# Performance work log

Measured on AMD Instinct MI355X. Metric: run time of the kernel, lower is better.

## Reference

```python
import jax, jax.numpy as jnp
import numpy as np

NC = 65536   # candidate centers across FPN levels (single image)
NP = 1024    # proposal boxes == points
D = 256      # points_feat_dim
C = 256      # in_channels (query/key dim)
START_LEVEL = 3
NEG = -1e30


def setup_inputs() -> dict:
    key = jax.random.key(0)
    ks = jax.random.split(key, 9)
    # centers: [y, x, size, stride]; stride in {8,16,32,64,128} -> lvl 0..4
    lvl = jax.random.randint(ks[0], (NC,), 0, 5)
    stride = (2.0 ** (lvl + START_LEVEL)).astype(jnp.float32)
    yx = jax.random.uniform(ks[1], (NC, 2), minval=0.0, maxval=1024.0)
    centers = jnp.concatenate([yx, stride[:, None], stride[:, None]], axis=1)
    # boxes: [x1, y1, x2, y2]
    x1y1 = jax.random.uniform(ks[2], (NP, 2), minval=0.0, maxval=900.0)
    wh = jax.random.uniform(ks[3], (NP, 2), minval=64.0, maxval=256.0)
    boxes = jnp.concatenate([x1y1, x1y1 + wh], axis=1)
    points_feat = jax.random.normal(ks[4], (NP, D), dtype=jnp.float32)
    box_feat = jax.random.normal(ks[5], (NC, D), dtype=jnp.float32)
    Wq = jax.random.normal(ks[6], (D, C), dtype=jnp.float32) / np.sqrt(D).astype(np.float32)
    bq = jnp.zeros((C,), dtype=jnp.float32)
    Wk = jax.random.normal(ks[7], (D, C), dtype=jnp.float32) / np.sqrt(D).astype(np.float32)
    bk = jnp.zeros((C,), dtype=jnp.float32)
    scales = 1.0 + 0.1 * jax.random.normal(ks[8], (5,), dtype=jnp.float32)
    return dict(points_feat=points_feat, box_feat=box_feat, centers=centers,
                boxes=boxes, Wq=Wq, bq=bq, Wk=Wk, bk=bk, scales=scales)


def reference(points_feat, box_feat, centers, boxes, Wq, bq, Wk, bk, scales):
    # geometry -> containment mask [NC, NP] (center c inside box p)
    coord = centers[:, :2] + jnp.floor_divide(centers[:, 2:3], 2.0)  # [NC,2]
    ys, xs = coord[:, 0], coord[:, 1]
    l = xs[:, None] - boxes[None, :, 0]
    t = ys[:, None] - boxes[None, :, 1]
    r = boxes[None, :, 2] - xs[:, None]
    b = boxes[None, :, 3] - ys[:, None]
    mask = jnp.minimum(jnp.minimum(l, t), jnp.minimum(r, b)) > 0     # [NC,NP]

    stride = centers[:, 3]
    lvl = (jnp.log2(stride) - START_LEVEL).astype(jnp.int32)         # [NC] in 0..4
    w = scales[lvl]                                                  # per-level scale

    query = points_feat @ Wq + bq                                    # [NP,C]
    keyf = (box_feat * w[:, None]) @ Wk + bk                         # [NC,C]

    sim = jnp.clip(keyf @ query.T, -50.0, 50.0)                      # [NC,NP]
    logits = jnp.where(mask, sim, NEG)
    attn = jax.nn.softmax(logits, axis=0)
    attn = jnp.where(mask, attn, 0.0)                                # zero out invalid
    merge = attn.T @ box_feat                                        # [NP,D]
    return points_feat + merge
```

## Files before the change

kernel.cpp:

```cpp
#include <hip/hip_runtime.h>

typedef unsigned short ushort_t;
typedef _Float16 half8 __attribute__((ext_vector_type(8)));
typedef short short8 __attribute__((ext_vector_type(8)));
typedef float floatx4 __attribute__((ext_vector_type(4)));

#define NCC 65536
#define NPP 1024
#define DD 256
#define NCHUNK 64
#define VROW 36
#define VTILE_B (256 * VROW * 2)

static __device__ __forceinline__ ushort_t f2h_bits(float x) {
  _Float16 h = (_Float16)x;
  return __builtin_bit_cast(ushort_t, h);
}
static __device__ __forceinline__ ushort_t f2bf_bits(float x) {
  unsigned u = __builtin_bit_cast(unsigned, x);
  unsigned r = (u + 0x7FFFu + ((u >> 16) & 1u)) >> 16;
  return (ushort_t)r;
}

static __device__ __forceinline__ void dma16(const void* g, void* l) {
  __builtin_amdgcn_global_load_lds((const __attribute__((address_space(1))) unsigned int*)g,
                                   (__attribute__((address_space(3))) unsigned int*)l, 16, 0, 0);
}

static __device__ __forceinline__ short8 mk_s8(uint2 lo, uint2 hi) {
  uint4 u;
  u.x = lo.x; u.y = lo.y; u.z = hi.x; u.w = hi.y;
  return __builtin_bit_cast(short8, u);
}

__global__ __launch_bounds__(256) void wt_prep(const float* __restrict__ Wq,
                                               const float* __restrict__ Wk,
                                               ushort_t* __restrict__ WqT,
                                               ushort_t* __restrict__ WkT) {
  __shared__ __align__(16) ushort_t lt[64][80];
  const float* W = blockIdx.y ? Wk : Wq;
  ushort_t* WT = blockIdx.y ? WkT : WqT;
  const int k0 = ((int)blockIdx.x & 3) * 64, n0 = ((int)blockIdx.x >> 2) * 64;
  const int t = threadIdx.x;
#pragma unroll
  for (int i = 0; i < 4; i++) {
    int f = t + 256 * i;
    int k = f >> 4, j = (f & 15) * 4;
    const float4 v = *(const float4*)&W[(size_t)(k0 + k) * DD + n0 + j];
    lt[j + 0][k] = f2h_bits(v.x);
    lt[j + 1][k] = f2h_bits(v.y);
    lt[j + 2][k] = f2h_bits(v.z);
    lt[j + 3][k] = f2h_bits(v.w);
  }
  __syncthreads();
#pragma unroll
  for (int i = 0; i < 2; i++) {
    int f = t + 256 * i;
    int nl = f >> 3, grp = f & 7;
    int n = n0 + nl;
    int kp = k0 + ((grp ^ (n & 7)) * 8);
    *(uint4*)&WT[(size_t)n * DD + kp] = *(const uint4*)&lt[nl][grp * 8];
  }
}

__global__ __launch_bounds__(256) void prep_gemm(
    const float* __restrict__ box_feat, const float* __restrict__ points_feat,
    const float* __restrict__ centers, const float* __restrict__ scales,
    const ushort_t* __restrict__ WqT, const ushort_t* __restrict__ WkT,
    const float* __restrict__ bq, const float* __restrict__ bk,
    ushort_t* __restrict__ q_out, ushort_t* __restrict__ kf_out,
    float2* __restrict__ xy) {
  __shared__ __align__(16) ushort_t lds_a[64][264];
  __shared__ __align__(16) ushort_t lds_b[64 * 256];
  __shared__ __align__(16) ushort_t lds_o[64][72];
  __shared__ float lds_s[64];

  const int t = threadIdx.x;
  const bool isQ = (blockIdx.x >= (NCC / 64));
  const int row0 = isQ ? ((int)blockIdx.x - NCC / 64) * 64 : (int)blockIdx.x * 64;
  const float* In = isQ ? points_feat : box_feat;
  const ushort_t* WT = isQ ? WqT : WkT;
  const float* Bi = isQ ? bq : bk;
  ushort_t* Out = isQ ? q_out : kf_out;
  const int swz = isQ ? 0 : 7;

  if (t < 64) {
    float s = 1.0f;
    if (!isQ) {
      int c = row0 + t;
      float stride = centers[c * 4 + 3];
      int lvl = (int)(log2f(stride) + 0.5f) - 3;
      lvl = lvl < 0 ? 0 : (lvl > 4 ? 4 : lvl);
      s = scales[lvl];
      float hf = floorf(centers[c * 4 + 2] * 0.5f);
      xy[c] = make_float2(centers[c * 4 + 1] + hf, centers[c * 4 + 0] + hf);
    }
    lds_s[t] = s;
  }
  __syncthreads();

#pragma unroll
  for (int i = 0; i < 16; i++) {
    int f = t + 256 * i;
    int r = f >> 6;
    int c4 = (f & 63) * 4;
    const float4 v = *(const float4*)&In[(size_t)(row0 + r) * DD + c4];
    float s = lds_s[r];
    ushort_t h0 = f2h_bits(v.x * s), h1 = f2h_bits(v.y * s);
    ushort_t h2 = f2h_bits(v.z * s), h3 = f2h_bits(v.w * s);
    *(uint2*)&lds_a[r][c4] =
        make_uint2((unsigned)h0 | ((unsigned)h1 << 16), (unsigned)h2 | ((unsigned)h3 << 16));
  }

  const int w = t >> 6, lane = t & 63, qd = lane >> 4, n = lane & 15;
  const int sw8 = (n & 7) * 8;

  for (int g = 0; g < 4; ++g) {
    __syncthreads();
#pragma unroll
    for (int j = 0; j < 8; ++j) {
      int sg = w * 8 + j;
      dma16(&WT[(size_t)g * 64 * DD + sg * 512 + lane * 8], &lds_b[sg * 512 + lane * 8]);
    }
    __syncthreads();

    floatx4 acc[4] = {};
#pragma unroll
    for (int s = 0; s < 8; s++) {
      half8 af = __builtin_bit_cast(half8, *(const uint4*)&lds_a[w * 16 + n][s * 32 + qd * 8]);
      int off = (s * 32 + qd * 8) ^ sw8;
#pragma unroll
      for (int nt = 0; nt < 4; ++nt) {
        half8 bf = __builtin_bit_cast(half8, *(const uint4*)&lds_b[(nt * 16 + n) * 256 + off]);
        acc[nt] = __builtin_amdgcn_mfma_f32_16x16x32_f16(af, bf, acc[nt], 0, 0, 0);
      }
    }
#pragma unroll
    for (int nt = 0; nt < 4; ++nt) {
      float b = Bi[g * 64 + nt * 16 + n];
#pragma unroll
      for (int r = 0; r < 4; r++) lds_o[w * 16 + qd * 4 + r][nt * 16 + n] = f2h_bits(acc[nt][r] + b);
    }
    __syncthreads();
#pragma unroll
    for (int i = 0; i < 2; i++) {
      int idx = t * 2 + i;
      int r = idx >> 3, grp = idx & 7;
      uint4 v = *(const uint4*)&lds_o[r][grp * 8];
      int grpS = grp ^ (swz & (r & 7));
      *(uint4*)&Out[(size_t)(row0 + r) * DD + (g * 8 + grpS) * 8] = v;
    }
  }
}

__global__ __launch_bounds__(256) void transpose_v(const float* __restrict__ box_feat,
                                                   ushort_t* __restrict__ vTb) {
  __shared__ __align__(16) ushort_t lt[64][72];
  const int t = threadIdx.x;
  const int c0 = blockIdx.x * 64, d0 = blockIdx.y * 64;
#pragma unroll
  for (int i = 0; i < 4; i++) {
    int f = t + 256 * i;
    int c = f >> 4;
    int j = (f & 15) * 4;
    const float4 v = *(const float4*)&box_feat[(size_t)(c0 + c) * DD + d0 + j];
    lt[j + 0][c] = f2bf_bits(v.x);
    lt[j + 1][c] = f2bf_bits(v.y);
    lt[j + 2][c] = f2bf_bits(v.z);
    lt[j + 3][c] = f2bf_bits(v.w);
  }
  __syncthreads();
#pragma unroll
  for (int i = 0; i < 2; i++) {
    int f = t + 256 * i;
    int d = f >> 3, j = f & 7;
    int tile = (c0 >> 5) + (j >> 2);
    size_t ob = (size_t)tile * (256 * VROW) + (size_t)(d0 + d) * VROW + (j & 3) * 8;
    const uint2* src = (const uint2*)&lt[d][j * 8];
    *(uint2*)&vTb[ob] = src[0];
    *(uint2*)&vTb[ob + 4] = src[1];
  }
}

template <bool PART>
__global__ __launch_bounds__(256, 2) void attn_kernel(
    const ushort_t* __restrict__ qf16, const ushort_t* __restrict__ kf16,
    const ushort_t* __restrict__ vTb, const float2* __restrict__ xy,
    const float* __restrict__ boxes, float* __restrict__ acc_out,
    float* __restrict__ den_out) {
  __shared__ __align__(16) ushort_t lds_k[2][32 * 256];
  __shared__ __align__(16) ushort_t lds_v[2][256 * VROW];
  __shared__ __align__(16) ushort_t lds_p[4][32][VROW];

  const int t = threadIdx.x;
  const int w = t >> 6, lane = t & 63, qd = lane >> 4, n = lane & 15;
  const int chunk = blockIdx.x;
  const int p0w = blockIdx.y * 128 + w * 32;
  const int cchunk = chunk * 1024;
  const int sw16 = (n & 7) * 16;

  half8 qfr[2][8];
  float4 bxv[2];
#pragma unroll
  for (int pt = 0; pt < 2; ++pt) {
    int p = p0w + pt * 16 + n;
#pragma unroll
    for (int s = 0; s < 8; s++)
      qfr[pt][s] =
          __builtin_bit_cast(half8, *(const uint4*)&qf16[(size_t)p * DD + s * 32 + qd * 8]);
    bxv[pt] = *(const float4*)&boxes[p * 4];
  }

  floatx4 macc[2][16] = {};
  float dsum0 = 0.f, dsum1 = 0.f;

  auto stage = [&](int it, int buf) {
    const size_t kbase = (size_t)(cchunk + it * 32) * DD * 2;
#pragma unroll
    for (int j = 0; j < 4; ++j) {
      int i = w * 4 + j;
      dma16((const char*)kf16 + kbase + i * 1024 + lane * 16,
            (char*)lds_k[buf] + i * 1024 + lane * 16);
    }
    const size_t vbase = (size_t)((cchunk >> 5) + it) * VTILE_B;
#pragma unroll
    for (int j = 0; j < 4; ++j) {
      int i = j * 4 + w;
      dma16((const char*)vTb + vbase + i * 1024 + lane * 16,
            (char*)lds_v[buf] + i * 1024 + lane * 16);
    }
    if (w < 2) {
      int i = 16 + w;
      dma16((const char*)vTb + vbase + i * 1024 + lane * 16,
            (char*)lds_v[buf] + i * 1024 + lane * 16);
    }
  };

  stage(0, 0);

  for (int it = 0; it < 32; ++it) {
    const int buf = it & 1;
    const int cb = cchunk + it * 32;
    __syncthreads();
    if (it + 1 < 32) stage(it + 1, buf ^ 1);

#pragma unroll
    for (int t2 = 0; t2 < 2; ++t2) {
      const char* krow = (const char*)lds_k[buf] + (t2 * 16 + n) * 512;
      floatx4 a0 = {}, a1 = {};
#pragma unroll
      for (int s = 0; s < 8; s++) {
        half8 af = __builtin_bit_cast(half8, *(const uint4*)(krow + ((s * 64 + qd * 16) ^ sw16)));
        a0 = __builtin_amdgcn_mfma_f32_16x16x32_f16(af, qfr[0][s], a0, 0, 0, 0);
        a1 = __builtin_amdgcn_mfma_f32_16x16x32_f16(af, qfr[1][s], a1, 0, 0, 0);
      }
      unsigned pk00 = 0, pk01 = 0, pk10 = 0, pk11 = 0;
#pragma unroll
      for (int r = 0; r < 4; r++) {
        int cl = t2 * 16 + qd * 4 + r;
        float2 pxy = xy[cb + cl];
        {
          float mn = fminf(fminf(pxy.x - bxv[0].x, pxy.y - bxv[0].y),
                           fminf(bxv[0].z - pxy.x, bxv[0].w - pxy.y));
          float sim = fminf(fmaxf(a0[r], -50.f), 50.f);
          float e = (mn > 0.f) ? exp2f((sim - 50.f) * 1.44269504f) : 0.f;
          dsum0 += e;
          unsigned b = (unsigned)f2bf_bits(e);
          if (r == 0) pk00 = b;
          else if (r == 1) pk00 |= b << 16;
          else if (r == 2) pk01 = b;
          else pk01 |= b << 16;
        }
        {
          float mn = fminf(fminf(pxy.x - bxv[1].x, pxy.y - bxv[1].y),
                           fminf(bxv[1].z - pxy.x, bxv[1].w - pxy.y));
          float sim = fminf(fmaxf(a1[r], -50.f), 50.f);
          float e = (mn > 0.f) ? exp2f((sim - 50.f) * 1.44269504f) : 0.f;
          dsum1 += e;
          unsigned b = (unsigned)f2bf_bits(e);
          if (r == 0) pk10 = b;
          else if (r == 1) pk10 |= b << 16;
          else if (r == 2) pk11 = b;
          else pk11 |= b << 16;
        }
      }
      *(uint2*)&lds_p[w][n][t2 * 16 + qd * 4] = make_uint2(pk00, pk01);
      *(uint2*)&lds_p[w][16 + n][t2 * 16 + qd * 4] = make_uint2(pk10, pk11);
    }
    __asm__ volatile("s_waitcnt lgkmcnt(0)" ::: "memory");

    const char* pr0 = (const char*)&lds_p[w][n][0];
    const char* pr1 = (const char*)&lds_p[w][16 + n][0];
    short8 a20 = mk_s8(*(const uint2*)(pr0 + qd * 16), *(const uint2*)(pr0 + qd * 16 + 8));
    short8 a21 = mk_s8(*(const uint2*)(pr1 + qd * 16), *(const uint2*)(pr1 + qd * 16 + 8));
#pragma unroll
    for (int dt = 0; dt < 16; ++dt) {
      const char* vrow = (const char*)lds_v[buf] + (dt * 16 + n) * (VROW * 2);
      short8 b2 = mk_s8(*(const uint2*)(vrow + qd * 16), *(const uint2*)(vrow + qd * 16 + 8));
      macc[0][dt] = __builtin_amdgcn_mfma_f32_16x16x32_bf16(a20, b2, macc[0][dt], 0, 0, 0);
      macc[1][dt] = __builtin_amdgcn_mfma_f32_16x16x32_bf16(a21, b2, macc[1][dt], 0, 0, 0);
    }
  }

  dsum0 += __shfl_xor(dsum0, 16, 64);
  dsum0 += __shfl_xor(dsum0, 32, 64);
  dsum1 += __shfl_xor(dsum1, 16, 64);
  dsum1 += __shfl_xor(dsum1, 32, 64);

  if (PART) {
    if (lane < 16) {
      den_out[(size_t)chunk * NPP + p0w + n] = dsum0;
      den_out[(size_t)chunk * NPP + p0w + 16 + n] = dsum1;
    }
    float* ab = acc_out + (size_t)chunk * NPP * DD;
#pragma unroll
    for (int pt = 0; pt < 2; ++pt)
#pragma unroll
      for (int dt = 0; dt < 16; ++dt)
#pragma unroll
        for (int r = 0; r < 4; r++)
          ab[(size_t)(p0w + pt * 16 + qd * 4 + r) * DD + dt * 16 + n] = macc[pt][dt][r];
  } else {
    if (lane < 16) {
      atomicAdd(&den_out[p0w + n], dsum0);
      atomicAdd(&den_out[p0w + 16 + n], dsum1);
    }
#pragma unroll
    for (int pt = 0; pt < 2; ++pt)
#pragma unroll
      for (int dt = 0; dt < 16; ++dt)
#pragma unroll
        for (int r = 0; r < 4; r++)
          atomicAdd(&acc_out[(size_t)(p0w + pt * 16 + qd * 4 + r) * DD + dt * 16 + n],
                    macc[pt][dt][r]);
  }
}

__global__ __launch_bounds__(256) void reduce_finalize(const float* __restrict__ points_feat,
                                                       const float* __restrict__ acc_part,
                                                       const float* __restrict__ den_part,
                                                       float* __restrict__ out) {
  const int p = blockIdx.x, t = threadIdx.x;
  float s = 0.f;
#pragma unroll 4
  for (int c = 0; c < NCHUNK; ++c) s += acc_part[((size_t)c * NPP + p) * DD + t];
  float dn = den_part[(size_t)(t & 63) * NPP + p];
#pragma unroll
  for (int o = 1; o < 64; o <<= 1) dn += __shfl_xor(dn, o, 64);
  float m = (dn > 0.f) ? s / dn : 0.f;
  out[(size_t)p * DD + t] = points_feat[(size_t)p * DD + t] + m;
}

__global__ void finalize(const float* __restrict__ points_feat, const float* __restrict__ acc,
                         const float* __restrict__ den, float* __restrict__ out) {
  int p = blockIdx.x, d = threadIdx.x;
  float dn = den[p];
  float m = (dn > 0.f) ? acc[p * DD + d] / dn : 0.f;
  out[p * DD + d] = points_feat[p * DD + d] + m;
}

extern "C" void kernel_launch(void* const* d_in, const int* in_sizes, int n_in, void* d_out,
                              int out_size, void* d_ws, size_t ws_size, hipStream_t stream) {
  const float* points_feat = (const float*)d_in[0];
  const float* box_feat = (const float*)d_in[1];
  const float* centers = (const float*)d_in[2];
  const float* boxes = (const float*)d_in[3];
  const float* Wq = (const float*)d_in[4];
  const float* bq = (const float*)d_in[5];
  const float* Wk = (const float*)d_in[6];
  const float* bk = (const float*)d_in[7];
  const float* scales = (const float*)d_in[8];

  char* p = (char*)d_ws;
  ushort_t* ws_q = (ushort_t*)p;        p += (size_t)NPP * DD * 2;
  ushort_t* ws_kf = (ushort_t*)p;       p += (size_t)NCC * DD * 2;
  ushort_t* ws_vTb = (ushort_t*)p;      p += (size_t)(NCC / 32) * VTILE_B;
  float2* ws_xy = (float2*)p;           p += (size_t)NCC * 8;
  ushort_t* ws_wqT = (ushort_t*)p;      p += (size_t)DD * DD * 2;
  ushort_t* ws_wkT = (ushort_t*)p;      p += (size_t)DD * DD * 2;
  float* ws_den = (float*)p;            p += (size_t)NCHUNK * NPP * 4;
  float* ws_acc = (float*)p;
  size_t need_part = (size_t)(p - (char*)d_ws) + (size_t)NCHUNK * NPP * DD * 4;
  const bool part = ws_size >= need_part;

  wt_prep<<<dim3(16, 2), 256, 0, stream>>>(Wq, Wk, ws_wqT, ws_wkT);
  prep_gemm<<<NCC / 64 + NPP / 64, 256, 0, stream>>>(box_feat, points_feat, centers, scales,
                                                     ws_wqT, ws_wkT, bq, bk, ws_q, ws_kf, ws_xy);
  transpose_v<<<dim3(NCC / 64, DD / 64), 256, 0, stream>>>(box_feat, ws_vTb);
  if (part) {
    attn_kernel<true><<<dim3(NCHUNK, 8), 256, 0, stream>>>(ws_q, ws_kf, ws_vTb, ws_xy, boxes,
                                                           ws_acc, ws_den);
    reduce_finalize<<<NPP, 256, 0, stream>>>(points_feat, ws_acc, ws_den, (float*)d_out);
  } else {
    hipMemsetAsync(ws_den, 0, ((size_t)NPP * DD + NPP) * sizeof(float), stream);
    float* acc1 = ws_den + NPP;
    attn_kernel<false><<<dim3(NCHUNK, 8), 256, 0, stream>>>(ws_q, ws_kf, ws_vTb, ws_xy, boxes,
                                                            acc1, ws_den);
    finalize<<<NPP, DD, 0, stream>>>(points_feat, acc1, ws_den, (float*)d_out);
  }
}
```

Baseline: 282.2 us.

## Pre-pack K and weights in MFMA fragment layout and load them directly from global

The weight and key matrices are now written in MFMA-fragment order, so the GEMM and attention kernels read operand fragments straight from global memory instead of staging swizzled tiles through LDS. The query is pre-scaled by log2(e), which lets the softmax exponent become a single clamp and exp2, and the redundant lower clip is dropped. VROW is widened to 40 so P and V fragments can be read with single 16-byte LDS loads, and per-tile center coordinates are prefetched into LDS with the V tiles. The trade-off is that every wave in a block now fetches the same K fragments from cache rather than sharing one LDS copy, and V tiles grow slightly.

```diff
diff --git a/kernel.cpp b/kernel.cpp
--- a/kernel.cpp
+++ b/kernel.cpp
@@ -9,8 +9,9 @@
 #define NPP 1024
 #define DD 256
 #define NCHUNK 64
-#define VROW 36
+#define VROW 40
 #define VTILE_B (256 * VROW * 2)
+#define CLIPL 72.134752f
 
 static __device__ __forceinline__ ushort_t f2h_bits(float x) {
   _Float16 h = (_Float16)x;
@@ -27,19 +28,13 @@
                                    (__attribute__((address_space(3))) unsigned int*)l, 16, 0, 0);
 }
 
-static __device__ __forceinline__ short8 mk_s8(uint2 lo, uint2 hi) {
-  uint4 u;
-  u.x = lo.x; u.y = lo.y; u.z = hi.x; u.w = hi.y;
-  return __builtin_bit_cast(short8, u);
-}
-
 __global__ __launch_bounds__(256) void wt_prep(const float* __restrict__ Wq,
                                                const float* __restrict__ Wk,
-                                               ushort_t* __restrict__ WqT,
-                                               ushort_t* __restrict__ WkT) {
-  __shared__ __align__(16) ushort_t lt[64][80];
+                                               ushort_t* __restrict__ WqF,
+                                               ushort_t* __restrict__ WkF) {
+  __shared__ __align__(16) ushort_t lt[64][72];
   const float* W = blockIdx.y ? Wk : Wq;
-  ushort_t* WT = blockIdx.y ? WkT : WqT;
+  ushort_t* WF = blockIdx.y ? WkF : WqF;
   const int k0 = ((int)blockIdx.x & 3) * 64, n0 = ((int)blockIdx.x >> 2) * 64;
   const int t = threadIdx.x;
 #pragma unroll
@@ -53,25 +48,26 @@
     lt[j + 3][k] = f2h_bits(v.w);
   }
   __syncthreads();
+  const int g = n0 >> 6;
 #pragma unroll
   for (int i = 0; i < 2; i++) {
     int f = t + 256 * i;
-    int nl = f >> 3, grp = f & 7;
-    int n = n0 + nl;
-    int kp = k0 + ((grp ^ (n & 7)) * 8);
-    *(uint4*)&WT[(size_t)n * DD + kp] = *(const uint4*)&lt[nl][grp * 8];
+    int nt = f >> 7, s_l = (f >> 6) & 1, ln = f & 63;
+    int qd = ln >> 4, nn = ln & 15;
+    uint4 v = *(const uint4*)&lt[nt * 16 + nn][s_l * 32 + qd * 8];
+    size_t slot = ((size_t)(g * 4 + nt) * 8 + (k0 >> 5) + s_l) * 64 + ln;
+    *(uint4*)&WF[slot * 8] = v;
   }
 }
 
 __global__ __launch_bounds__(256) void prep_gemm(
     const float* __restrict__ box_feat, const float* __restrict__ points_feat,
     const float* __restrict__ centers, const float* __restrict__ scales,
-    const ushort_t* __restrict__ WqT, const ushort_t* __restrict__ WkT,
+    const ushort_t* __restrict__ WqF, const ushort_t* __restrict__ WkF,
     const float* __restrict__ bq, const float* __restrict__ bk,
-    ushort_t* __restrict__ q_out, ushort_t* __restrict__ kf_out,
+    ushort_t* __restrict__ q_out, ushort_t* __restrict__ kfA,
     float2* __restrict__ xy) {
   __shared__ __align__(16) ushort_t lds_a[64][264];
-  __shared__ __align__(16) ushort_t lds_b[64 * 256];
   __shared__ __align__(16) ushort_t lds_o[64][72];
   __shared__ float lds_s[64];
 
@@ -79,10 +75,8 @@
   const bool isQ = (blockIdx.x >= (NCC / 64));
   const int row0 = isQ ? ((int)blockIdx.x - NCC / 64) * 64 : (int)blockIdx.x * 64;
   const float* In = isQ ? points_feat : box_feat;
-  const ushort_t* WT = isQ ? WqT : WkT;
+  const ushort_t* WF = isQ ? WqF : WkF;
   const float* Bi = isQ ? bq : bk;
-  ushort_t* Out = isQ ? q_out : kf_out;
-  const int swz = isQ ? 0 : 7;
 
   if (t < 64) {
     float s = 1.0f;
@@ -111,44 +105,52 @@
     *(uint2*)&lds_a[r][c4] =
         make_uint2((unsigned)h0 | ((unsigned)h1 << 16), (unsigned)h2 | ((unsigned)h3 << 16));
   }
+  __syncthreads();
 
   const int w = t >> 6, lane = t & 63, qd = lane >> 4, n = lane & 15;
-  const int sw8 = (n & 7) * 8;
 
   for (int g = 0; g < 4; ++g) {
-    __syncthreads();
-#pragma unroll
-    for (int j = 0; j < 8; ++j) {
-      int sg = w * 8 + j;
-      dma16(&WT[(size_t)g * 64 * DD + sg * 512 + lane * 8], &lds_b[sg * 512 + lane * 8]);
-    }
-    __syncthreads();
-
     floatx4 acc[4] = {};
 #pragma unroll
     for (int s = 0; s < 8; s++) {
       half8 af = __builtin_bit_cast(half8, *(const uint4*)&lds_a[w * 16 + n][s * 32 + qd * 8]);
-      int off = (s * 32 + qd * 8) ^ sw8;
 #pragma unroll
       for (int nt = 0; nt < 4; ++nt) {
-        half8 bf = __builtin_bit_cast(half8, *(const uint4*)&lds_b[(nt * 16 + n) * 256 + off]);
+        half8 bf = __builtin_bit_cast(
+            half8, *(const uint4*)&WF[(((size_t)(g * 4 + nt) * 8 + s) * 64 + lane) * 8]);
         acc[nt] = __builtin_amdgcn_mfma_f32_16x16x32_f16(af, bf, acc[nt], 0, 0, 0);
       }
     }
+    __syncthreads();
 #pragma unroll
     for (int nt = 0; nt < 4; ++nt) {
       float b = Bi[g * 64 + nt * 16 + n];
 #pragma unroll
-      for (int r = 0; r < 4; r++) lds_o[w * 16 + qd * 4 + r][nt * 16 + n] = f2h_bits(acc[nt][r] + b);
+      for (int r = 0; r < 4; r++) {
+        float v = acc[nt][r] + b;
+        if (isQ) v *= 1.44269504f;
+        lds_o[w * 16 + qd * 4 + r][nt * 16 + n] = f2h_bits(v);
+      }
     }
     __syncthreads();
-#pragma unroll
-    for (int i = 0; i < 2; i++) {
-      int idx = t * 2 + i;
-      int r = idx >> 3, grp = idx & 7;
-      uint4 v = *(const uint4*)&lds_o[r][grp * 8];
-      int grpS = grp ^ (swz & (r & 7));
-      *(uint4*)&Out[(size_t)(row0 + r) * DD + (g * 8 + grpS) * 8] = v;
+    if (isQ) {
+#pragma unroll
+      for (int i = 0; i < 2; i++) {
+        int f = t + 256 * i;
+        int r = f >> 3, grp = f & 7;
+        *(uint4*)&q_out[(size_t)(row0 + r) * DD + g * 64 + grp * 8] =
+            *(const uint4*)&lds_o[r][grp * 8];
+      }
+    } else {
+#pragma unroll
+      for (int i = 0; i < 2; i++) {
+        int f = t + 256 * i;
+        int ct = f >> 7, s_l = (f >> 6) & 1, ln = f & 63;
+        int lqd = ln >> 4, lnn = ln & 15;
+        uint4 v = *(const uint4*)&lds_o[ct * 16 + lnn][s_l * 32 + lqd * 8];
+        size_t slot = ((size_t)((row0 >> 4) + ct) * 8 + g * 2 + s_l) * 64 + ln;
+        *(uint4*)&kfA[slot * 8] = v;
+      }
     }
   }
 }
@@ -176,28 +178,25 @@
     int d = f >> 3, j = f & 7;
     int tile = (c0 >> 5) + (j >> 2);
     size_t ob = (size_t)tile * (256 * VROW) + (size_t)(d0 + d) * VROW + (j & 3) * 8;
-    const uint2* src = (const uint2*)&lt[d][j * 8];
-    *(uint2*)&vTb[ob] = src[0];
-    *(uint2*)&vTb[ob + 4] = src[1];
+    *(uint4*)&vTb[ob] = *(const uint4*)&lt[d][j * 8];
   }
 }
 
 template <bool PART>
 __global__ __launch_bounds__(256, 2) void attn_kernel(
-    const ushort_t* __restrict__ qf16, const ushort_t* __restrict__ kf16,
+    const ushort_t* __restrict__ qf16, const ushort_t* __restrict__ kfA,
     const ushort_t* __restrict__ vTb, const float2* __restrict__ xy,
     const float* __restrict__ boxes, float* __restrict__ acc_out,
     float* __restrict__ den_out) {
-  __shared__ __align__(16) ushort_t lds_k[2][32 * 256];
   __shared__ __align__(16) ushort_t lds_v[2][256 * VROW];
   __shared__ __align__(16) ushort_t lds_p[4][32][VROW];
+  __shared__ __align__(16) float2 lds_xy[2][32];
 
   const int t = threadIdx.x;
   const int w = t >> 6, lane = t & 63, qd = lane >> 4, n = lane & 15;
   const int chunk = blockIdx.x;
   const int p0w = blockIdx.y * 128 + w * 32;
   const int cchunk = chunk * 1024;
-  const int sw16 = (n & 7) * 16;
 
   half8 qfr[2][8];
   float4 bxv[2];
@@ -214,43 +213,34 @@
   floatx4 macc[2][16] = {};
   float dsum0 = 0.f, dsum1 = 0.f;
 
-  auto stage = [&](int it, int buf) {
-    const size_t kbase = (size_t)(cchunk + it * 32) * DD * 2;
-#pragma unroll
-    for (int j = 0; j < 4; ++j) {
-      int i = w * 4 + j;
-      dma16((const char*)kf16 + kbase + i * 1024 + lane * 16,
-            (char*)lds_k[buf] + i * 1024 + lane * 16);
-    }
-    const size_t vbase = (size_t)((cchunk >> 5) + it) * VTILE_B;
-#pragma unroll
-    for (int j = 0; j < 4; ++j) {
-      int i = j * 4 + w;
-      dma16((const char*)vTb + vbase + i * 1024 + lane * 16,
-            (char*)lds_v[buf] + i * 1024 + lane * 16);
-    }
-    if (w < 2) {
-      int i = 16 + w;
-      dma16((const char*)vTb + vbase + i * 1024 + lane * 16,
-            (char*)lds_v[buf] + i * 1024 + lane * 16);
-    }
+  auto stage = [&](int it2, int b) {
+    const char* src = (const char*)vTb + ((size_t)(cchunk >> 5) + it2) * VTILE_B;
+    char* dst = (char*)lds_v[b];
+#pragma unroll
+    for (int jj = 0; jj < 5; ++jj) {
+      int i = w * 5 + jj;
+      dma16(src + i * 1024 + lane * 16, dst + i * 1024 + lane * 16);
+    }
+    if (w == 0 && lane < 16)
+      dma16((const char*)xy + ((size_t)cchunk + it2 * 32) * 8 + lane * 16,
+            (char*)lds_xy[b] + lane * 16);
   };
 
   stage(0, 0);
 
   for (int it = 0; it < 32; ++it) {
     const int buf = it & 1;
-    const int cb = cchunk + it * 32;
     __syncthreads();
     if (it + 1 < 32) stage(it + 1, buf ^ 1);
 
+    const size_t tbase = (size_t)(cchunk >> 4) + it * 2;
 #pragma unroll
     for (int t2 = 0; t2 < 2; ++t2) {
-      const char* krow = (const char*)lds_k[buf] + (t2 * 16 + n) * 512;
+      const ushort_t* kb = kfA + (tbase + t2) * 4096;
       floatx4 a0 = {}, a1 = {};
 #pragma unroll
       for (int s = 0; s < 8; s++) {
-        half8 af = __builtin_bit_cast(half8, *(const uint4*)(krow + ((s * 64 + qd * 16) ^ sw16)));
+        half8 af = __builtin_bit_cast(half8, *(const uint4*)&kb[(s * 64 + lane) * 8]);
         a0 = __builtin_amdgcn_mfma_f32_16x16x32_f16(af, qfr[0][s], a0, 0, 0, 0);
         a1 = __builtin_amdgcn_mfma_f32_16x16x32_f16(af, qfr[1][s], a1, 0, 0, 0);
       }
@@ -258,12 +248,12 @@
 #pragma unroll
       for (int r = 0; r < 4; r++) {
         int cl = t2 * 16 + qd * 4 + r;
-        float2 pxy = xy[cb + cl];
+        float2 pxy = lds_xy[buf][cl];
         {
           float mn = fminf(fminf(pxy.x - bxv[0].x, pxy.y - bxv[0].y),
                            fminf(bxv[0].z - pxy.x, bxv[0].w - pxy.y));
-          float sim = fminf(fmaxf(a0[r], -50.f), 50.f);
-          float e = (mn > 0.f) ? exp2f((sim - 50.f) * 1.44269504f) : 0.f;
+          float simL = fminf(a0[r], CLIPL);
+          float e = (mn > 0.f) ? exp2f(simL - CLIPL) : 0.f;
           dsum0 += e;
           unsigned b = (unsigned)f2bf_bits(e);
           if (r == 0) pk00 = b;
@@ -274,8 +264,8 @@
         {
           float mn = fminf(fminf(pxy.x - bxv[1].x, pxy.y - bxv[1].y),
                            fminf(bxv[1].z - pxy.x, bxv[1].w - pxy.y));
-          float sim = fminf(fmaxf(a1[r], -50.f), 50.f);
-          float e = (mn > 0.f) ? exp2f((sim - 50.f) * 1.44269504f) : 0.f;
+          float simL = fminf(a1[r], CLIPL);
+          float e = (mn > 0.f) ? exp2f(simL - CLIPL) : 0.f;
           dsum1 += e;
           unsigned b = (unsigned)f2bf_bits(e);
           if (r == 0) pk10 = b;
@@ -289,14 +279,12 @@
     }
     __asm__ volatile("s_waitcnt lgkmcnt(0)" ::: "memory");
 
-    const char* pr0 = (const char*)&lds_p[w][n][0];
-    const char* pr1 = (const char*)&lds_p[w][16 + n][0];
-    short8 a20 = mk_s8(*(const uint2*)(pr0 + qd * 16), *(const uint2*)(pr0 + qd * 16 + 8));
-    short8 a21 = mk_s8(*(const uint2*)(pr1 + qd * 16), *(const uint2*)(pr1 + qd * 16 + 8));
+    short8 a20 = __builtin_bit_cast(short8, *(const uint4*)&lds_p[w][n][qd * 8]);
+    short8 a21 = __builtin_bit_cast(short8, *(const uint4*)&lds_p[w][16 + n][qd * 8]);
 #pragma unroll
     for (int dt = 0; dt < 16; ++dt) {
-      const char* vrow = (const char*)lds_v[buf] + (dt * 16 + n) * (VROW * 2);
-      short8 b2 = mk_s8(*(const uint2*)(vrow + qd * 16), *(const uint2*)(vrow + qd * 16 + 8));
+      short8 b2 =
+          __builtin_bit_cast(short8, *(const uint4*)&lds_v[buf][(dt * 16 + n) * VROW + qd * 8]);
       macc[0][dt] = __builtin_amdgcn_mfma_f32_16x16x32_bf16(a20, b2, macc[0][dt], 0, 0, 0);
       macc[1][dt] = __builtin_amdgcn_mfma_f32_16x16x32_bf16(a21, b2, macc[1][dt], 0, 0, 0);
     }
@@ -372,29 +360,29 @@
   const float* scales = (const float*)d_in[8];
 
   char* p = (char*)d_ws;
-  ushort_t* ws_q = (ushort_t*)p;        p += (size_t)NPP * DD * 2;
-  ushort_t* ws_kf = (ushort_t*)p;       p += (size_t)NCC * DD * 2;
-  ushort_t* ws_vTb = (ushort_t*)p;      p += (size_t)(NCC / 32) * VTILE_B;
-  float2* ws_xy = (float2*)p;           p += (size_t)NCC * 8;
-  ushort_t* ws_wqT = (ushort_t*)p;      p += (size_t)DD * DD * 2;
-  ushort_t* ws_wkT = (ushort_t*)p;      p += (size_t)DD * DD * 2;
-  float* ws_den = (float*)p;            p += (size_t)NCHUNK * NPP * 4;
+  ushort_t* ws_q = (ushort_t*)p;    p += (size_t)NPP * DD * 2;
+  ushort_t* ws_kfA = (ushort_t*)p;  p += (size_t)NCC * DD * 2;
+  ushort_t* ws_vTb = (ushort_t*)p;  p += (size_t)(NCC / 32) * VTILE_B;
+  float2* ws_xy = (float2*)p;       p += (size_t)NCC * 8;
+  ushort_t* ws_wqF = (ushort_t*)p;  p += (size_t)DD * DD * 2;
+  ushort_t* ws_wkF = (ushort_t*)p;  p += (size_t)DD * DD * 2;
+  float* ws_den = (float*)p;        p += (size_t)NCHUNK * NPP * 4;
   float* ws_acc = (float*)p;
   size_t need_part = (size_t)(p - (char*)d_ws) + (size_t)NCHUNK * NPP * DD * 4;
   const bool part = ws_size >= need_part;
 
-  wt_prep<<<dim3(16, 2), 256, 0, stream>>>(Wq, Wk, ws_wqT, ws_wkT);
+  wt_prep<<<dim3(16, 2), 256, 0, stream>>>(Wq, Wk, ws_wqF, ws_wkF);
   prep_gemm<<<NCC / 64 + NPP / 64, 256, 0, stream>>>(box_feat, points_feat, centers, scales,
-                                                     ws_wqT, ws_wkT, bq, bk, ws_q, ws_kf, ws_xy);
+                                                     ws_wqF, ws_wkF, bq, bk, ws_q, ws_kfA, ws_xy);
   transpose_v<<<dim3(NCC / 64, DD / 64), 256, 0, stream>>>(box_feat, ws_vTb);
   if (part) {
-    attn_kernel<true><<<dim3(NCHUNK, 8), 256, 0, stream>>>(ws_q, ws_kf, ws_vTb, ws_xy, boxes,
+    attn_kernel<true><<<dim3(NCHUNK, 8), 256, 0, stream>>>(ws_q, ws_kfA, ws_vTb, ws_xy, boxes,
                                                            ws_acc, ws_den);
     reduce_finalize<<<NPP, 256, 0, stream>>>(points_feat, ws_acc, ws_den, (float*)d_out);
   } else {
     hipMemsetAsync(ws_den, 0, ((size_t)NPP * DD + NPP) * sizeof(float), stream);
     float* acc1 = ws_den + NPP;
-    attn_kernel<false><<<dim3(NCHUNK, 8), 256, 0, stream>>>(ws_q, ws_kf, ws_vTb, ws_xy, boxes,
+    attn_kernel<false><<<dim3(NCHUNK, 8), 256, 0, stream>>>(ws_q, ws_kfA, ws_vTb, ws_xy, boxes,
                                                             acc1, ws_den);
     finalize<<<NPP, DD, 0, stream>>>(points_feat, acc1, ws_den, (float*)d_out);
   }
```

Result: slower. 343.1 us (+21.6%).

## Fold Wq/Wk into per-point bilinear form, skip key projection GEMM

Applied to the files above, without the earlier changes.

Rewrites the similarity algebraically: instead of projecting all 65536 box features through Wk, it precomputes Wk·Wq^T and then G = points_feat·(Wk Wq^T), so sim is box_feat·G^T, with the per-level scale and bias terms folded into per-center and per-point scalars. This removes the large key-projection GEMM and merges the V transpose and center metadata into one pass over box_feat. The softmax shift now uses the clip bound, applied through a fused FMA and a min before exp2. The partial accumulators are also stored in bf16 to halve reduction traffic. In exchange, the fp16 weight product and the bf16 partials lose some precision.

```diff
diff --git a/kernel.cpp b/kernel.cpp
--- a/kernel.cpp
+++ b/kernel.cpp
@@ -11,6 +11,8 @@
 #define NCHUNK 64
 #define VROW 36
 #define VTILE_B (256 * VROW * 2)
+#define L2E 1.44269504f
+#define CLIPL 72.134752f
 
 static __device__ __forceinline__ ushort_t f2h_bits(float x) {
   _Float16 h = (_Float16)x;
@@ -21,176 +23,168 @@
   unsigned r = (u + 0x7FFFu + ((u >> 16) & 1u)) >> 16;
   return (ushort_t)r;
 }
-
+static __device__ __forceinline__ float bf2f(ushort_t b) {
+  unsigned u = ((unsigned)b) << 16;
+  return __builtin_bit_cast(float, u);
+}
+static __device__ __forceinline__ half8 cvt8(const float* p) {
+  float4 a = *(const float4*)p, b = *(const float4*)(p + 4);
+  half8 h;
+  h[0] = (_Float16)a.x; h[1] = (_Float16)a.y; h[2] = (_Float16)a.z; h[3] = (_Float16)a.w;
+  h[4] = (_Float16)b.x; h[5] = (_Float16)b.y; h[6] = (_Float16)b.z; h[7] = (_Float16)b.w;
+  return h;
+}
 static __device__ __forceinline__ void dma16(const void* g, void* l) {
   __builtin_amdgcn_global_load_lds((const __attribute__((address_space(1))) unsigned int*)g,
                                    (__attribute__((address_space(3))) unsigned int*)l, 16, 0, 0);
 }
-
 static __device__ __forceinline__ short8 mk_s8(uint2 lo, uint2 hi) {
   uint4 u;
   u.x = lo.x; u.y = lo.y; u.z = hi.x; u.w = hi.y;
   return __builtin_bit_cast(short8, u);
 }
 
-__global__ __launch_bounds__(256) void wt_prep(const float* __restrict__ Wq,
+__global__ __launch_bounds__(256) void mk_prep(const float* __restrict__ Wq,
                                                const float* __restrict__ Wk,
-                                               ushort_t* __restrict__ WqT,
-                                               ushort_t* __restrict__ WkT) {
-  __shared__ __align__(16) ushort_t lt[64][80];
-  const float* W = blockIdx.y ? Wk : Wq;
-  ushort_t* WT = blockIdx.y ? WkT : WqT;
-  const int k0 = ((int)blockIdx.x & 3) * 64, n0 = ((int)blockIdx.x >> 2) * 64;
+                                               const float* __restrict__ bq,
+                                               const float* __restrict__ bk,
+                                               ushort_t* __restrict__ Mk, float* __restrict__ tu,
+                                               float* __restrict__ tv, float* __restrict__ s0v) {
   const int t = threadIdx.x;
-#pragma unroll
-  for (int i = 0; i < 4; i++) {
-    int f = t + 256 * i;
-    int k = f >> 4, j = (f & 15) * 4;
-    const float4 v = *(const float4*)&W[(size_t)(k0 + k) * DD + n0 + j];
-    lt[j + 0][k] = f2h_bits(v.x);
-    lt[j + 1][k] = f2h_bits(v.y);
-    lt[j + 2][k] = f2h_bits(v.z);
-    lt[j + 3][k] = f2h_bits(v.w);
-  }
+  if (blockIdx.x == 16) {
+    float su = 0.f, sv = 0.f;
+    for (int j = 0; j < DD; j += 4) {
+      float4 a = *(const float4*)&Wk[(size_t)t * DD + j];
+      float4 b = *(const float4*)&bq[j];
+      su += a.x * b.x + a.y * b.y + a.z * b.z + a.w * b.w;
+      float4 c = *(const float4*)&Wq[(size_t)t * DD + j];
+      float4 d = *(const float4*)&bk[j];
+      sv += c.x * d.x + c.y * d.y + c.z * d.z + c.w * d.w;
+    }
+    tu[t] = su;
+    tv[t] = sv;
+    __shared__ float red[256];
+    red[t] = bk[t] * bq[t];
+    __syncthreads();
+    for (int o = 128; o; o >>= 1) {
+      if (t < o) red[t] += red[t + o];
+      __syncthreads();
+    }
+    if (t == 0) s0v[0] = red[0];
+    return;
+  }
+  const int m0 = ((int)blockIdx.x & 3) * 64, e0 = ((int)blockIdx.x >> 2) * 64;
+  const int w = t >> 6, lane = t & 63, qd = lane >> 4, n = lane & 15;
+  floatx4 acc[4] = {};
+#pragma unroll
+  for (int s = 0; s < 8; s++) {
+    half8 af = cvt8(&Wk[(size_t)(m0 + w * 16 + n) * DD + s * 32 + qd * 8]);
+#pragma unroll
+    for (int nt = 0; nt < 4; ++nt) {
+      half8 bf = cvt8(&Wq[(size_t)(e0 + nt * 16 + n) * DD + s * 32 + qd * 8]);
+      acc[nt] = __builtin_amdgcn_mfma_f32_16x16x32_f16(af, bf, acc[nt], 0, 0, 0);
+    }
+  }
+#pragma unroll
+  for (int nt = 0; nt < 4; ++nt)
+#pragma unroll
+    for (int r = 0; r < 4; r++)
+      Mk[(size_t)(m0 + w * 16 + qd * 4 + r) * DD + e0 + nt * 16 + n] = f2h_bits(acc[nt][r]);
+}
+
+__global__ __launch_bounds__(256) void gt_prep(const float* __restrict__ pf,
+                                               const ushort_t* __restrict__ Mk,
+                                               const float* __restrict__ tv,
+                                               const float* __restrict__ s0v,
+                                               ushort_t* __restrict__ Gt,
+                                               float* __restrict__ gamma) {
+  const int t = threadIdx.x, p0 = (int)blockIdx.x * 64;
+  const int w = t >> 6, lane = t & 63, qd = lane >> 4, n = lane & 15;
+  floatx4 acc[16] = {};
+#pragma unroll
+  for (int s = 0; s < 8; s++) {
+    half8 af = cvt8(&pf[(size_t)(p0 + w * 16 + n) * DD + s * 32 + qd * 8]);
+#pragma unroll
+    for (int nt = 0; nt < 16; ++nt) {
+      half8 bf = __builtin_bit_cast(half8,
+                                    *(const uint4*)&Mk[(size_t)(nt * 16 + n) * DD + s * 32 + qd * 8]);
+      acc[nt] = __builtin_amdgcn_mfma_f32_16x16x32_f16(af, bf, acc[nt], 0, 0, 0);
+    }
+  }
+#pragma unroll
+  for (int nt = 0; nt < 16; ++nt)
+#pragma unroll
+    for (int r = 0; r < 4; r++)
+      Gt[(size_t)(p0 + w * 16 + qd * 4 + r) * DD + nt * 16 + n] = f2h_bits(acc[nt][r]);
+  if (t < 64) {
+    float s = s0v[0];
+    for (int j = 0; j < DD; j += 4) {
+      float4 a = *(const float4*)&pf[(size_t)(p0 + t) * DD + j];
+      float4 b = *(const float4*)&tv[j];
+      s += a.x * b.x + a.y * b.y + a.z * b.z + a.w * b.w;
+    }
+    gamma[p0 + t] = s * L2E - CLIPL;
+  }
+}
+
+__global__ __launch_bounds__(256) void bt_prep(const float* __restrict__ bf,
+                                               const float* __restrict__ centers,
+                                               const float* __restrict__ scales,
+                                               const float* __restrict__ tu,
+                                               ushort_t* __restrict__ bfR,
+                                               ushort_t* __restrict__ vTb,
+                                               float4* __restrict__ meta) {
+  __shared__ float tu_s[256];
+  __shared__ __align__(16) ushort_t lt[256][40];
+  const int t = threadIdx.x, c0 = (int)blockIdx.x * 32;
+  tu_s[t] = tu[t];
   __syncthreads();
-#pragma unroll
-  for (int i = 0; i < 2; i++) {
-    int f = t + 256 * i;
-    int nl = f >> 3, grp = f & 7;
-    int n = n0 + nl;
-    int kp = k0 + ((grp ^ (n & 7)) * 8);
-    *(uint4*)&WT[(size_t)n * DD + kp] = *(const uint4*)&lt[nl][grp * 8];
-  }
-}
-
-__global__ __launch_bounds__(256) void prep_gemm(
-    const float* __restrict__ box_feat, const float* __restrict__ points_feat,
-    const float* __restrict__ centers, const float* __restrict__ scales,
-    const ushort_t* __restrict__ WqT, const ushort_t* __restrict__ WkT,
-    const float* __restrict__ bq, const float* __restrict__ bk,
-    ushort_t* __restrict__ q_out, ushort_t* __restrict__ kf_out,
-    float2* __restrict__ xy) {
-  __shared__ __align__(16) ushort_t lds_a[64][264];
-  __shared__ __align__(16) ushort_t lds_b[64 * 256];
-  __shared__ __align__(16) ushort_t lds_o[64][72];
-  __shared__ float lds_s[64];
-
-  const int t = threadIdx.x;
-  const bool isQ = (blockIdx.x >= (NCC / 64));
-  const int row0 = isQ ? ((int)blockIdx.x - NCC / 64) * 64 : (int)blockIdx.x * 64;
-  const float* In = isQ ? points_feat : box_feat;
-  const ushort_t* WT = isQ ? WqT : WkT;
-  const float* Bi = isQ ? bq : bk;
-  ushort_t* Out = isQ ? q_out : kf_out;
-  const int swz = isQ ? 0 : 7;
-
-  if (t < 64) {
-    float s = 1.0f;
-    if (!isQ) {
-      int c = row0 + t;
-      float stride = centers[c * 4 + 3];
-      int lvl = (int)(log2f(stride) + 0.5f) - 3;
-      lvl = lvl < 0 ? 0 : (lvl > 4 ? 4 : lvl);
-      s = scales[lvl];
-      float hf = floorf(centers[c * 4 + 2] * 0.5f);
-      xy[c] = make_float2(centers[c * 4 + 1] + hf, centers[c * 4 + 0] + hf);
-    }
-    lds_s[t] = s;
+  const int c = t >> 3, sub = t & 7;
+  float du = 0.f;
+#pragma unroll
+  for (int i = 0; i < 8; i++) {
+    int f4 = sub + 8 * i;
+    int d0 = f4 * 4;
+    float4 v = *(const float4*)&bf[(size_t)(c0 + c) * DD + d0];
+    du += v.x * tu_s[d0] + v.y * tu_s[d0 + 1] + v.z * tu_s[d0 + 2] + v.w * tu_s[d0 + 3];
+    int l = f4 >> 1;
+    int u = (l & ~7) | ((l & 7) ^ (c & 7));
+    ushort_t h0 = f2h_bits(v.x), h1 = f2h_bits(v.y), h2 = f2h_bits(v.z), h3 = f2h_bits(v.w);
+    *(uint2*)&bfR[(size_t)(c0 + c) * DD + u * 8 + (d0 & 7)] =
+        make_uint2((unsigned)h0 | ((unsigned)h1 << 16), (unsigned)h2 | ((unsigned)h3 << 16));
+    lt[d0 + 0][c] = f2bf_bits(v.x);
+    lt[d0 + 1][c] = f2bf_bits(v.y);
+    lt[d0 + 2][c] = f2bf_bits(v.z);
+    lt[d0 + 3][c] = f2bf_bits(v.w);
+  }
+  du += __shfl_xor(du, 1, 64);
+  du += __shfl_xor(du, 2, 64);
+  du += __shfl_xor(du, 4, 64);
+  if (sub == 0) {
+    const float4 ce = *(const float4*)&centers[(size_t)(c0 + c) * 4];
+    int lvl = (int)(log2f(ce.w) + 0.5f) - 3;
+    lvl = lvl < 0 ? 0 : (lvl > 4 ? 4 : lvl);
+    float wsc = scales[lvl];
+    float hf = floorf(ce.z * 0.5f);
+    meta[c0 + c] = make_float4(wsc * L2E, wsc * du * L2E, ce.y + hf, ce.x + hf);
   }
   __syncthreads();
-
-#pragma unroll
-  for (int i = 0; i < 16; i++) {
-    int f = t + 256 * i;
-    int r = f >> 6;
-    int c4 = (f & 63) * 4;
-    const float4 v = *(const float4*)&In[(size_t)(row0 + r) * DD + c4];
-    float s = lds_s[r];
-    ushort_t h0 = f2h_bits(v.x * s), h1 = f2h_bits(v.y * s);
-    ushort_t h2 = f2h_bits(v.z * s), h3 = f2h_bits(v.w * s);
-    *(uint2*)&lds_a[r][c4] =
-        make_uint2((unsigned)h0 | ((unsigned)h1 << 16), (unsigned)h2 | ((unsigned)h3 << 16));
-  }
-
-  const int w = t >> 6, lane = t & 63, qd = lane >> 4, n = lane & 15;
-  const int sw8 = (n & 7) * 8;
-
-  for (int g = 0; g < 4; ++g) {
-    __syncthreads();
-#pragma unroll
-    for (int j = 0; j < 8; ++j) {
-      int sg = w * 8 + j;
-      dma16(&WT[(size_t)g * 64 * DD + sg * 512 + lane * 8], &lds_b[sg * 512 + lane * 8]);
-    }
-    __syncthreads();
-
-    floatx4 acc[4] = {};
-#pragma unroll
-    for (int s = 0; s < 8; s++) {
-      half8 af = __builtin_bit_cast(half8, *(const uint4*)&lds_a[w * 16 + n][s * 32 + qd * 8]);
-      int off = (s * 32 + qd * 8) ^ sw8;
-#pragma unroll
-      for (int nt = 0; nt < 4; ++nt) {
-        half8 bf = __builtin_bit_cast(half8, *(const uint4*)&lds_b[(nt * 16 + n) * 256 + off]);
-        acc[nt] = __builtin_amdgcn_mfma_f32_16x16x32_f16(af, bf, acc[nt], 0, 0, 0);
-      }
-    }
-#pragma unroll
-    for (int nt = 0; nt < 4; ++nt) {
-      float b = Bi[g * 64 + nt * 16 + n];
-#pragma unroll
-      for (int r = 0; r < 4; r++) lds_o[w * 16 + qd * 4 + r][nt * 16 + n] = f2h_bits(acc[nt][r] + b);
-    }
-    __syncthreads();
-#pragma unroll
-    for (int i = 0; i < 2; i++) {
-      int idx = t * 2 + i;
-      int r = idx >> 3, grp = idx & 7;
-      uint4 v = *(const uint4*)&lds_o[r][grp * 8];
-      int grpS = grp ^ (swz & (r & 7));
-      *(uint4*)&Out[(size_t)(row0 + r) * DD + (g * 8 + grpS) * 8] = v;
-    }
-  }
-}
-
-__global__ __launch_bounds__(256) void transpose_v(const float* __restrict__ box_feat,
-                                                   ushort_t* __restrict__ vTb) {
-  __shared__ __align__(16) ushort_t lt[64][72];
-  const int t = threadIdx.x;
-  const int c0 = blockIdx.x * 64, d0 = blockIdx.y * 64;
-#pragma unroll
-  for (int i = 0; i < 4; i++) {
-    int f = t + 256 * i;
-    int c = f >> 4;
-    int j = (f & 15) * 4;
-    const float4 v = *(const float4*)&box_feat[(size_t)(c0 + c) * DD + d0 + j];
-    lt[j + 0][c] = f2bf_bits(v.x);
-    lt[j + 1][c] = f2bf_bits(v.y);
-    lt[j + 2][c] = f2bf_bits(v.z);
-    lt[j + 3][c] = f2bf_bits(v.w);
-  }
-  __syncthreads();
-#pragma unroll
-  for (int i = 0; i < 2; i++) {
-    int f = t + 256 * i;
-    int d = f >> 3, j = f & 7;
-    int tile = (c0 >> 5) + (j >> 2);
-    size_t ob = (size_t)tile * (256 * VROW) + (size_t)(d0 + d) * VROW + (j & 3) * 8;
-    const uint2* src = (const uint2*)&lt[d][j * 8];
-    *(uint2*)&vTb[ob] = src[0];
-    *(uint2*)&vTb[ob + 4] = src[1];
-  }
+  char* dst = (char*)vTb + (size_t)blockIdx.x * VTILE_B + (size_t)t * (VROW * 2);
+  const char* src = (const char*)&lt[t][0];
+#pragma unroll
+  for (int i = 0; i < 9; i++) *(uint2*)(dst + i * 8) = *(const uint2*)(src + i * 8);
 }
 
 template <bool PART>
 __global__ __launch_bounds__(256, 2) void attn_kernel(
-    const ushort_t* __restrict__ qf16, const ushort_t* __restrict__ kf16,
-    const ushort_t* __restrict__ vTb, const float2* __restrict__ xy,
-    const float* __restrict__ boxes, float* __restrict__ acc_out,
-    float* __restrict__ den_out) {
+    const ushort_t* __restrict__ Gt, const float* __restrict__ gamma,
+    const ushort_t* __restrict__ bfR, const ushort_t* __restrict__ vTb,
+    const float4* __restrict__ meta, const float* __restrict__ boxes,
+    void* __restrict__ acc_out, float* __restrict__ den_out) {
   __shared__ __align__(16) ushort_t lds_k[2][32 * 256];
   __shared__ __align__(16) ushort_t lds_v[2][256 * VROW];
   __shared__ __align__(16) ushort_t lds_p[4][32][VROW];
+  __shared__ __align__(16) float4 lds_m[2][32];
 
   const int t = threadIdx.x;
   const int w = t >> 6, lane = t & 63, qd = lane >> 4, n = lane & 15;
@@ -199,48 +193,50 @@
   const int cchunk = chunk * 1024;
   const int sw16 = (n & 7) * 16;
 
-  half8 qfr[2][8];
+  half8 gfr[2][8];
   float4 bxv[2];
+  float gam[2];
 #pragma unroll
   for (int pt = 0; pt < 2; ++pt) {
     int p = p0w + pt * 16 + n;
 #pragma unroll
     for (int s = 0; s < 8; s++)
-      qfr[pt][s] =
-          __builtin_bit_cast(half8, *(const uint4*)&qf16[(size_t)p * DD + s * 32 + qd * 8]);
-    bxv[pt] = *(const float4*)&boxes[p * 4];
+      gfr[pt][s] = __builtin_bit_cast(half8, *(const uint4*)&Gt[(size_t)p * DD + s * 32 + qd * 8]);
+    bxv[pt] = *(const float4*)&boxes[(size_t)p * 4];
+    gam[pt] = gamma[p];
   }
 
   floatx4 macc[2][16] = {};
   float dsum0 = 0.f, dsum1 = 0.f;
 
-  auto stage = [&](int it, int buf) {
-    const size_t kbase = (size_t)(cchunk + it * 32) * DD * 2;
+  auto stage = [&](int it2, int b) {
+    const char* ks = (const char*)bfR + (size_t)(cchunk + it2 * 32) * 512;
+    char* kd = (char*)lds_k[b];
 #pragma unroll
     for (int j = 0; j < 4; ++j) {
       int i = w * 4 + j;
-      dma16((const char*)kf16 + kbase + i * 1024 + lane * 16,
-            (char*)lds_k[buf] + i * 1024 + lane * 16);
-    }
-    const size_t vbase = (size_t)((cchunk >> 5) + it) * VTILE_B;
+      dma16(ks + i * 1024 + lane * 16, kd + i * 1024 + lane * 16);
+    }
+    const char* vs = (const char*)vTb + ((size_t)(cchunk >> 5) + it2) * VTILE_B;
+    char* vd = (char*)lds_v[b];
 #pragma unroll
     for (int j = 0; j < 4; ++j) {
       int i = j * 4 + w;
-      dma16((const char*)vTb + vbase + i * 1024 + lane * 16,
-            (char*)lds_v[buf] + i * 1024 + lane * 16);
+      dma16(vs + i * 1024 + lane * 16, vd + i * 1024 + lane * 16);
     }
     if (w < 2) {
       int i = 16 + w;
-      dma16((const char*)vTb + vbase + i * 1024 + lane * 16,
-            (char*)lds_v[buf] + i * 1024 + lane * 16);
-    }
+      dma16(vs + i * 1024 + lane * 16, vd + i * 1024 + lane * 16);
+    }
+    if (w == 0 && lane < 32)
+      dma16((const char*)meta + (size_t)(cchunk + it2 * 32) * 16 + lane * 16,
+            (char*)lds_m[b] + lane * 16);
   };
 
   stage(0, 0);
 
   for (int it = 0; it < 32; ++it) {
     const int buf = it & 1;
-    const int cb = cchunk + it * 32;
     __syncthreads();
     if (it + 1 < 32) stage(it + 1, buf ^ 1);
 
@@ -251,19 +247,19 @@
 #pragma unroll
       for (int s = 0; s < 8; s++) {
         half8 af = __builtin_bit_cast(half8, *(const uint4*)(krow + ((s * 64 + qd * 16) ^ sw16)));
-        a0 = __builtin_amdgcn_mfma_f32_16x16x32_f16(af, qfr[0][s], a0, 0, 0, 0);
-        a1 = __builtin_amdgcn_mfma_f32_16x16x32_f16(af, qfr[1][s], a1, 0, 0, 0);
+        a0 = __builtin_amdgcn_mfma_f32_16x16x32_f16(af, gfr[0][s], a0, 0, 0, 0);
+        a1 = __builtin_amdgcn_mfma_f32_16x16x32_f16(af, gfr[1][s], a1, 0, 0, 0);
       }
       unsigned pk00 = 0, pk01 = 0, pk10 = 0, pk11 = 0;
 #pragma unroll
       for (int r = 0; r < 4; r++) {
         int cl = t2 * 16 + qd * 4 + r;
-        float2 pxy = xy[cb + cl];
+        float4 mt = lds_m[buf][cl];
         {
-          float mn = fminf(fminf(pxy.x - bxv[0].x, pxy.y - bxv[0].y),
-                           fminf(bxv[0].z - pxy.x, bxv[0].w - pxy.y));
-          float sim = fminf(fmaxf(a0[r], -50.f), 50.f);
-          float e = (mn > 0.f) ? exp2f((sim - 50.f) * 1.44269504f) : 0.f;
+          float mn = fminf(fminf(mt.z - bxv[0].x, mt.w - bxv[0].y),
+                           fminf(bxv[0].z - mt.z, bxv[0].w - mt.w));
+          float targ = fmaf(mt.x, a0[r], mt.y) + gam[0];
+          float e = (mn > 0.f) ? exp2f(fminf(targ, 0.f)) : 0.f;
           dsum0 += e;
           unsigned b = (unsigned)f2bf_bits(e);
           if (r == 0) pk00 = b;
@@ -272,10 +268,10 @@
           else pk01 |= b << 16;
         }
         {
-          float mn = fminf(fminf(pxy.x - bxv[1].x, pxy.y - bxv[1].y),
-                           fminf(bxv[1].z - pxy.x, bxv[1].w - pxy.y));
-          float sim = fminf(fmaxf(a1[r], -50.f), 50.f);
-          float e = (mn > 0.f) ? exp2f((sim - 50.f) * 1.44269504f) : 0.f;
+          float mn = fminf(fminf(mt.z - bxv[1].x, mt.w - bxv[1].y),
+                           fminf(bxv[1].z - mt.z, bxv[1].w - mt.w));
+          float targ = fmaf(mt.x, a1[r], mt.y) + gam[1];
+          float e = (mn > 0.f) ? exp2f(fminf(targ, 0.f)) : 0.f;
           dsum1 += e;
           unsigned b = (unsigned)f2bf_bits(e);
           if (r == 0) pk10 = b;
@@ -312,38 +308,39 @@
       den_out[(size_t)chunk * NPP + p0w + n] = dsum0;
       den_out[(size_t)chunk * NPP + p0w + 16 + n] = dsum1;
     }
-    float* ab = acc_out + (size_t)chunk * NPP * DD;
+    ushort_t* ab = (ushort_t*)acc_out + (size_t)chunk * NPP * DD;
 #pragma unroll
     for (int pt = 0; pt < 2; ++pt)
 #pragma unroll
       for (int dt = 0; dt < 16; ++dt)
 #pragma unroll
         for (int r = 0; r < 4; r++)
-          ab[(size_t)(p0w + pt * 16 + qd * 4 + r) * DD + dt * 16 + n] = macc[pt][dt][r];
+          ab[(size_t)(p0w + pt * 16 + qd * 4 + r) * DD + dt * 16 + n] = f2bf_bits(macc[pt][dt][r]);
   } else {
     if (lane < 16) {
       atomicAdd(&den_out[p0w + n], dsum0);
       atomicAdd(&den_out[p0w + 16 + n], dsum1);
     }
+    float* ab = (float*)acc_out;
 #pragma unroll
     for (int pt = 0; pt < 2; ++pt)
 #pragma unroll
       for (int dt = 0; dt < 16; ++dt)
 #pragma unroll
         for (int r = 0; r < 4; r++)
-          atomicAdd(&acc_out[(size_t)(p0w + pt * 16 + qd * 4 + r) * DD + dt * 16 + n],
+          atomicAdd(&ab[(size_t)(p0w + pt * 16 + qd * 4 + r) * DD + dt * 16 + n],
                     macc[pt][dt][r]);
   }
 }
 
 __global__ __launch_bounds__(256) void reduce_finalize(const float* __restrict__ points_feat,
-                                                       const float* __restrict__ acc_part,
+                                                       const ushort_t* __restrict__ acc_part,
                                                        const float* __restrict__ den_part,
                                                        float* __restrict__ out) {
   const int p = blockIdx.x, t = threadIdx.x;
   float s = 0.f;
 #pragma unroll 4
-  for (int c = 0; c < NCHUNK; ++c) s += acc_part[((size_t)c * NPP + p) * DD + t];
+  for (int c = 0; c < NCHUNK; ++c) s += bf2f(acc_part[((size_t)c * NPP + p) * DD + t]);
   float dn = den_part[(size_t)(t & 63) * NPP + p];
 #pragma unroll
   for (int o = 1; o < 64; o <<= 1) dn += __shfl_xor(dn, o, 64);
@@ -372,30 +369,48 @@
   const float* scales = (const float*)d_in[8];
 
   char* p = (char*)d_ws;
-  ushort_t* ws_q = (ushort_t*)p;        p += (size_t)NPP * DD * 2;
-  ushort_t* ws_kf = (ushort_t*)p;       p += (size_t)NCC * DD * 2;
-  ushort_t* ws_vTb = (ushort_t*)p;      p += (size_t)(NCC / 32) * VTILE_B;
-  float2* ws_xy = (float2*)p;           p += (size_t)NCC * 8;
-  ushort_t* ws_wqT = (ushort_t*)p;      p += (size_t)DD * DD * 2;
-  ushort_t* ws_wkT = (ushort_t*)p;      p += (size_t)DD * DD * 2;
-  float* ws_den = (float*)p;            p += (size_t)NCHUNK * NPP * 4;
-  float* ws_acc = (float*)p;
-  size_t need_part = (size_t)(p - (char*)d_ws) + (size_t)NCHUNK * NPP * DD * 4;
-  const bool part = ws_size >= need_part;
-
-  wt_prep<<<dim3(16, 2), 256, 0, stream>>>(Wq, Wk, ws_wqT, ws_wkT);
-  prep_gemm<<<NCC / 64 + NPP / 64, 256, 0, stream>>>(box_feat, points_feat, centers, scales,
-                                                     ws_wqT, ws_wkT, bq, bk, ws_q, ws_kf, ws_xy);
-  transpose_v<<<dim3(NCC / 64, DD / 64), 256, 0, stream>>>(box_feat, ws_vTb);
-  if (part) {
-    attn_kernel<true><<<dim3(NCHUNK, 8), 256, 0, stream>>>(ws_q, ws_kf, ws_vTb, ws_xy, boxes,
-                                                           ws_acc, ws_den);
-    reduce_finalize<<<NPP, 256, 0, stream>>>(points_feat, ws_acc, ws_den, (float*)d_out);
+  ushort_t* ws_accP = (ushort_t*)p;  p += (size_t)NCHUNK * NPP * DD * 2;
+  float* ws_den = (float*)p;         p += (size_t)NCHUNK * NPP * 4;
+  ushort_t* ws_bfR = (ushort_t*)p;   p += (size_t)NCC * DD * 2;
+  ushort_t* ws_vTb = (ushort_t*)p;   p += (size_t)(NCC / 32) * VTILE_B;
+  ushort_t* ws_Gt = (ushort_t*)p;    p += (size_t)NPP * DD * 2;
+  float4* ws_meta = (float4*)p;      p += (size_t)NCC * 16;
+  float* ws_gamma = (float*)p;       p += (size_t)NPP * 4;
+  size_t need_part = (size_t)(p - (char*)d_ws);
+
+  if (ws_size >= need_part) {
+    ushort_t* ws_Mk = ws_accP;
+    float* ws_tu = (float*)(ws_Mk + (size_t)DD * DD);
+    float* ws_tv = ws_tu + DD;
+    float* ws_s0 = ws_tv + DD;
+
+    mk_prep<<<17, 256, 0, stream>>>(Wq, Wk, bq, bk, ws_Mk, ws_tu, ws_tv, ws_s0);
+    gt_prep<<<16, 256, 0, stream>>>(points_feat, ws_Mk, ws_tv, ws_s0, ws_Gt, ws_gamma);
+    bt_prep<<<NCC / 32, 256, 0, stream>>>(box_feat, centers, scales, ws_tu, ws_bfR, ws_vTb,
+                                          ws_meta);
+    attn_kernel<true><<<dim3(NCHUNK, 8), 256, 0, stream>>>(ws_Gt, ws_gamma, ws_bfR, ws_vTb,
+                                                           ws_meta, boxes, ws_accP, ws_den);
+    reduce_finalize<<<NPP, 256, 0, stream>>>(points_feat, ws_accP, ws_den, (float*)d_out);
   } else {
-    hipMemsetAsync(ws_den, 0, ((size_t)NPP * DD + NPP) * sizeof(float), stream);
-    float* acc1 = ws_den + NPP;
-    attn_kernel<false><<<dim3(NCHUNK, 8), 256, 0, stream>>>(ws_q, ws_kf, ws_vTb, ws_xy, boxes,
-                                                            acc1, ws_den);
-    finalize<<<NPP, DD, 0, stream>>>(points_feat, acc1, ws_den, (float*)d_out);
-  }
-}
+    char* q = (char*)d_ws;
+    ushort_t* f_bfR = (ushort_t*)q;  q += (size_t)NCC * DD * 2;
+    ushort_t* f_vTb = (ushort_t*)q;  q += (size_t)(NCC / 32) * VTILE_B;
+    ushort_t* f_Gt = (ushort_t*)q;   q += (size_t)NPP * DD * 2;
+    float4* f_meta = (float4*)q;     q += (size_t)NCC * 16;
+    float* f_gamma = (float*)q;      q += (size_t)NPP * 4;
+    float* f_den = (float*)q;        q += (size_t)NPP * 4;
+    float* f_acc = (float*)q;        q += (size_t)NPP * DD * 4;
+    ushort_t* f_Mk = (ushort_t*)f_acc;
+    float* f_tu = (float*)(f_Mk + (size_t)DD * DD);
+    float* f_tv = f_tu + DD;
+    float* f_s0 = f_tv + DD;
+
+    mk_prep<<<17, 256, 0, stream>>>(Wq, Wk, bq, bk, f_Mk, f_tu, f_tv, f_s0);
+    gt_prep<<<16, 256, 0, stream>>>(points_feat, f_Mk, f_tv, f_s0, f_Gt, f_gamma);
+    bt_prep<<<NCC / 32, 256, 0, stream>>>(box_feat, centers, scales, f_tu, f_bfR, f_vTb, f_meta);
+    hipMemsetAsync(f_den, 0, ((size_t)NPP * DD + NPP) * sizeof(float), stream);
+    attn_kernel<false><<<dim3(NCHUNK, 8), 256, 0, stream>>>(f_Gt, f_gamma, f_bfR, f_vTb, f_meta,
+                                                            boxes, f_acc, f_den);
+    finalize<<<NPP, DD, 0, stream>>>(points_feat, f_acc, f_den, (float*)d_out);
+  }
+}
```

New measurement: 299.3 us. 6.1% more time.
